# Performance work log

Hardware: AMD Instinct MI355X
Metric: run time of the kernel (lower is better)

The kernel has to match this reference:

```python
import jax, jax.numpy as jnp
import numpy as np

E = 16          # total experts (two halves of 8)
E_HALF = 8
K = 2           # top-k per token
CAP_FACTOR = 2  # expert capacity factor over the average load


def setup_inputs() -> dict:
    key = jax.random.key(0)
    ks = jax.random.split(key, 6)
    N, D, F = 16384, 1024, 1024  # tokens, d_model, d_ff (repo uses d_ff == d_model)
    s = 0.02
    return {
        "moe_inp": jax.random.normal(ks[0], (N, D), jnp.float32),
        "gate_w": jax.random.normal(ks[1], (D, E), jnp.float32) * s,   # gate Linear(d_model, 16)
        "gate_b": jnp.zeros((E,), jnp.float32),
        "route_w": jax.random.normal(ks[2], (D, 1), jnp.float32) * s,  # self.weights Linear(d_model, 1)
        "route_b": jnp.zeros((1,), jnp.float32),
        "W1": jax.random.normal(ks[3], (E, D, F), jnp.float32) * s,    # htoh4 per expert
        "b1": jnp.zeros((E, F), jnp.float32),
        "W2": jax.random.normal(ks[4], (E, F, D), jnp.float32) * s,    # h4toh per expert
        "b2": jnp.zeros((E, D), jnp.float32),
    }


def reference(moe_inp, gate_w, gate_b, route_w, route_b, W1, b1, W2, b2):
    N, D = moe_inp.shape
    # --- gate: logits over 16 experts; half 1 -> experts [0,8), half 2 -> experts [8,16)
    logits = moe_inp @ gate_w + gate_b                       # [N, E]
    val1, idx1 = jax.lax.top_k(logits[:, :E_HALF], K)        # [N, K]
    score1 = jax.nn.softmax(val1, axis=-1)
    val2, idx2 = jax.lax.top_k(logits[:, E_HALF:], K)
    score2 = jax.nn.softmax(val2, axis=-1)
    idx2 = idx2 + E_HALF                                     # shift into second expert range (gate_top_k_idx_2 + 8)
    # --- hard binary split of tokens via sigmoid(Linear(d,1)) > 0.5
    group1 = jax.nn.sigmoid(moe_inp @ route_w + route_b) > 0.5   # [N, 1]
    idx = jnp.where(group1, idx1, idx2)                      # [N, K] combined routing
    score = jnp.where(group1, score1, score2)                # [N, K]
    # --- dispatch: flatten (token, slot) pairs, capacity-bucket per expert
    T = N * K
    C = CAP_FACTOR * T // E                                  # expert capacity
    flat_idx = idx.reshape(-1)                               # [T]
    flat_x = jnp.repeat(moe_inp, K, axis=0)                  # [T, D]
    onehot = jax.nn.one_hot(flat_idx, E, dtype=jnp.int32)    # [T, E]
    pos_in_e = (jnp.cumsum(onehot, axis=0) * onehot).sum(axis=1) - 1  # [T] slot within expert
    valid = pos_in_e < C
    safe_pos = jnp.where(valid, pos_in_e, 0)
    buf = jnp.zeros((E, C, D), moe_inp.dtype).at[flat_idx, safe_pos].add(
        jnp.where(valid[:, None], flat_x, 0.0))              # [E, C, D] contiguous per-expert inputs
    # --- grouped expert FFN: relu(x W1 + b1) W2 + b2 (dropout = identity in eval)
    h = jax.nn.relu(jnp.einsum('ecd,edf->ecf', buf, W1) + b1[:, None, :])
    y = jnp.einsum('ecf,efd->ecd', h, W2) + b2[:, None, :]   # [E, C, D]
    # --- gather back and combine with gate scores
    y_flat = jnp.where(valid[:, None], y[flat_idx, safe_pos], 0.0)   # [T, D]
    out = (y_flat.reshape(N, K, D) * score[..., None]).sum(axis=1)   # [N, D]
    return out
```

## Files before the change

kernel.cpp:

```cpp
#include <hip/hip_runtime.h>
#include <hip/hip_bf16.h>
#include <stdint.h>

#define N_TOK 16384
#define DMODEL 1024
#define EXP 16
#define CAP 4096
#define TT 32768

typedef __bf16 bf16x8 __attribute__((ext_vector_type(8)));
typedef __bf16 bf16x4 __attribute__((ext_vector_type(4)));
typedef float  f32x4  __attribute__((ext_vector_type(4)));

__device__ __forceinline__ void gl_lds16(const void* g, void* s) {
  __builtin_amdgcn_global_load_lds(
      (__attribute__((address_space(1))) void*)(void*)g,
      (__attribute__((address_space(3))) void*)s, 16, 0, 0);
}

__device__ __forceinline__ float bfbits2f(unsigned short u) {
  return __uint_as_float(((unsigned)u) << 16);
}

#define FENCE asm volatile("" ::: "memory")
#define BAR() do { FENCE; __builtin_amdgcn_s_barrier(); FENCE; } while (0)

__global__ __launch_bounds__(256) void convw_kernel(const float* __restrict__ W1,
                                                    const float* __restrict__ W2,
                                                    __bf16* __restrict__ W1bt,
                                                    __bf16* __restrict__ W2bt) {
  __shared__ float tile[64][65];
  int b = blockIdx.x;
  int tx = b & 15;
  int ty = (b >> 4) & 15;
  int e  = (b >> 8) & 15;
  int which = (b >> 12) & 1;
  const float* src = (which ? W2 : W1) + (size_t)e * DMODEL * DMODEL;
  __bf16*      dst = (which ? W2bt : W1bt) + (size_t)e * DMODEL * DMODEL;
  int t = threadIdx.x;
  int r = t >> 2;
  int cs = (t & 3) * 16;
  int r0 = ty * 64, c0 = tx * 64;
  #pragma unroll
  for (int i = 0; i < 16; i += 4) {
    float4 v = *(const float4*)(src + (size_t)(r0 + r) * DMODEL + c0 + cs + i);
    tile[r][cs + i + 0] = v.x; tile[r][cs + i + 1] = v.y;
    tile[r][cs + i + 2] = v.z; tile[r][cs + i + 3] = v.w;
  }
  __syncthreads();
  bf16x8 o1, o2;
  #pragma unroll
  for (int i = 0; i < 8; i++) o1[i] = (__bf16)tile[cs + i][r];
  #pragma unroll
  for (int i = 0; i < 8; i++) o2[i] = (__bf16)tile[cs + 8 + i][r];
  *(bf16x8*)(dst + (size_t)(c0 + r) * DMODEL + r0 + cs)     = o1;
  *(bf16x8*)(dst + (size_t)(c0 + r) * DMODEL + r0 + cs + 8) = o2;
}

__global__ __launch_bounds__(256) void gate_kernel(const float* __restrict__ x,
                                                   const float* __restrict__ gw,
                                                   const float* __restrict__ gb,
                                                   const float* __restrict__ rw,
                                                   const float* __restrict__ rb,
                                                   int* __restrict__ idxo,
                                                   float* __restrict__ sco,
                                                   __bf16* __restrict__ Xb) {
  __shared__ float gws[512 * 17];
  __shared__ float rws[512];
  int tid = threadIdx.x;
  int w = tid >> 6, lane = tid & 63;
  int n = blockIdx.x * 4 + w;
  const float* xr = x + (size_t)n * DMODEL;
  __bf16* xbr = Xb + (size_t)n * DMODEL;

  float acc[17];
  #pragma unroll
  for (int j = 0; j < 17; j++) acc[j] = 0.f;

  for (int c = 0; c < 2; c++) {
    int c0 = c * 512;
    __syncthreads();
    for (int i = tid; i < 512 * 16; i += 256)
      gws[(i >> 4) * 17 + (i & 15)] = gw[c0 * 16 + i];
    for (int i = tid; i < 512; i += 256)
      rws[i] = rw[c0 + i];
    __syncthreads();

    float xv[8];
    #pragma unroll
    for (int u = 0; u < 8; u++) xv[u] = xr[c0 + u * 64 + lane];
    #pragma unroll
    for (int u = 0; u < 8; u++) xbr[c0 + u * 64 + lane] = (__bf16)xv[u];
    #pragma unroll
    for (int u = 0; u < 8; u++) {
      int dl = u * 64 + lane;
      const float* g = &gws[dl * 17];
      #pragma unroll
      for (int j = 0; j < 16; j++) acc[j] += xv[u] * g[j];
      acc[16] += xv[u] * rws[dl];
    }
  }

  #pragma unroll
  for (int o = 1; o < 64; o <<= 1) {
    #pragma unroll
    for (int j = 0; j < 17; j++) acc[j] += __shfl_xor(acc[j], o);
  }
  if (lane == 0) {
    float rv = acc[16] + rb[0];
    bool g1 = rv > 0.f;
    float c[8];
    #pragma unroll
    for (int j = 0; j < 8; j++)
      c[j] = (g1 ? acc[j] + gb[j] : acc[8 + j] + gb[8 + j]);
    int i1 = 0; float v1 = c[0];
    #pragma unroll
    for (int j = 1; j < 8; j++) { if (c[j] > v1) { v1 = c[j]; i1 = j; } }
    int i2 = -1; float v2 = -3.4e38f;
    #pragma unroll
    for (int j = 0; j < 8; j++) { if (j != i1 && c[j] > v2) { v2 = c[j]; i2 = j; } }
    float e2 = expf(v2 - v1);
    float den = 1.f + e2;
    int base = g1 ? 0 : 8;
    idxo[2 * n] = base + i1; idxo[2 * n + 1] = base + i2;
    sco[2 * n] = 1.f / den;  sco[2 * n + 1] = e2 / den;
  }
}

__global__ __launch_bounds__(1024) void scan_kernel(const int* __restrict__ idx,
                                                    float* __restrict__ sco,
                                                    int* __restrict__ rowlist,
                                                    int* __restrict__ cnt,
                                                    int* __restrict__ off) {
  __shared__ int hist[16 * 1024];
  int tid = threadIdx.x;
  #pragma unroll
  for (int e = 0; e < 16; e++) hist[e * 1024 + tid] = 0;
  __syncthreads();
  int base = tid * 32;
  for (int i = 0; i < 32; i++) {
    int e = idx[base + i];
    hist[e * 1024 + tid]++;
  }
  __syncthreads();
  int w = tid >> 6, lane = tid & 63;
  {
    int e = w;
    int running = 0;
    for (int cch = 0; cch < 16; cch++) {
      int v = hist[e * 1024 + cch * 64 + lane];
      int orig = v;
      #pragma unroll
      for (int o = 1; o < 64; o <<= 1) {
        int nv = __shfl_up(v, o);
        if (lane >= o) v += nv;
      }
      hist[e * 1024 + cch * 64 + lane] = running + v - orig;
      running += __shfl(v, 63);
    }
    if (lane == 0) cnt[e] = running;
  }
  __syncthreads();
  if (tid == 0) {
    int o = 0;
    for (int e = 0; e < 16; e++) {
      int c = cnt[e]; if (c > CAP) c = CAP;
      off[e] = o; cnt[e] = c; o += c;
    }
  }
  __syncthreads();
  for (int i = 0; i < 32; i++) {
    int t = base + i;
    int e = idx[t];
    int r = hist[e * 1024 + tid]++;
    if (r < CAP) rowlist[e * CAP + r] = t;
    else sco[t] = 0.f;
  }
}

#define GBM 256
#define GBN 256
#define GBK 64
#define NKT (DMODEL / GBK)

__global__ __launch_bounds__(512) void moe_gemm(const __bf16* __restrict__ A,
                                                const __bf16* __restrict__ Bt,
                                                const float* __restrict__ bias,
                                                __bf16* __restrict__ out,
                                                const int* __restrict__ rowlist,
                                                const int* __restrict__ cnt,
                                                const int* __restrict__ off,
                                                int mode) {
  __shared__ char lds[131072];
  int bx = blockIdx.x;
  int em = (bx & 7) * 32 + (bx >> 3);
  int e  = em >> 4;
  int m0 = (em & 15) * GBM;
  int ce = cnt[e];
  if (m0 >= ce) return;
  int n0 = blockIdx.y * GBN;
  int oe = off[e];
  int tid = threadIdx.x;

  const __bf16* aP[2][2];
  const __bf16* bP[2][2];
  #pragma unroll
  for (int h = 0; h < 2; h++)
    #pragma unroll
    for (int j = 0; j < 2; j++) {
      int lin = j * 512 + tid;
      int srow = lin >> 3;
      int gsrc = (lin & 7) ^ (srow & 7);
      int rr = m0 + h * 128 + srow; if (rr > ce - 1) rr = ce - 1;
      size_t arow;
      if (mode == 0) arow = (size_t)(rowlist[e * CAP + rr] >> 1);
      else           arow = (size_t)(oe + rr);
      aP[h][j] = A + arow * DMODEL + gsrc * 8;
      bP[h][j] = Bt + (size_t)e * DMODEL * DMODEL + (size_t)(n0 + h * 128 + srow) * DMODEL + gsrc * 8;
    }

  int w = tid >> 6, lane = tid & 63;
  int ah = w >> 2;
  int bh = (w & 3) >> 1;
  int bl = (w & 1) * 64;
  int fr = lane & 15, fg = lane >> 4;

  int aRd = ah * 16384 + fr * 128;
  int bRd = 65536 + bh * 16384 + (bl + fr) * 128;
  int gk0 = ((fg)     ^ (fr & 7)) * 16;
  int gk1 = ((4 | fg) ^ (fr & 7)) * 16;

  f32x4 acc[8][4];
  #pragma unroll
  for (int mi = 0; mi < 8; mi++)
    #pragma unroll
    for (int ni = 0; ni < 4; ni++)
      #pragma unroll
      for (int l = 0; l < 4; l++) acc[mi][ni][l] = 0.f;

  auto stA = [&](int s, int h) {
    char* dst = lds + (s & 1) * 32768 + h * 16384;
    gl_lds16(aP[h][0] + s * 64, dst + (size_t)tid * 16);
    gl_lds16(aP[h][1] + s * 64, dst + (size_t)(512 + tid) * 16);
  };
  auto stB = [&](int s, int h) {
    char* dst = lds + 65536 + (s & 1) * 32768 + h * 16384;
    gl_lds16(bP[h][0] + s * 64, dst + (size_t)tid * 16);
    gl_lds16(bP[h][1] + s * 64, dst + (size_t)(512 + tid) * 16);
  };

  stA(0, 0); stA(0, 1); stB(0, 0); stB(0, 1);
  stA(1, 0); stA(1, 1); stB(1, 0); stB(1, 1);
  asm volatile("s_waitcnt vmcnt(8)" ::: "memory");
  BAR();

  bf16x8 afA[4][2], bq0[2][2], bq1[2][2];
  for (int t = 0; t < NKT; ++t) {
    const char* Ab = lds + (t & 1) * 32768 + aRd;
    const char* Bb = lds + (t & 1) * 32768 + bRd;

    #pragma unroll
    for (int mi = 0; mi < 4; mi++) {
      afA[mi][0] = *(const bf16x8*)(Ab + mi * 2048 + gk0);
      afA[mi][1] = *(const bf16x8*)(Ab + mi * 2048 + gk1);
    }
    #pragma unroll
    for (int ni = 0; ni < 2; ni++) {
      bq0[ni][0] = *(const bf16x8*)(Bb + ni * 2048 + gk0);
      bq0[ni][1] = *(const bf16x8*)(Bb + ni * 2048 + gk1);
    }
    if (t >= 1 && t <= 14) stA(t + 1, 0);
    BAR();
    __builtin_amdgcn_s_setprio(1);
    #pragma unroll
    for (int kk = 0; kk < 2; kk++)
      #pragma unroll
      for (int mi = 0; mi < 4; mi++)
        #pragma unroll
        for (int ni = 0; ni < 2; ni++)
          acc[mi][ni] = __builtin_amdgcn_mfma_f32_16x16x32_bf16(afA[mi][kk], bq0[ni][kk], acc[mi][ni], 0, 0, 0);
    __builtin_amdgcn_s_setprio(0);
    BAR();

    #pragma unroll
    for (int ni = 0; ni < 2; ni++) {
      bq1[ni][0] = *(const bf16x8*)(Bb + (2 + ni) * 2048 + gk0);
      bq1[ni][1] = *(const bf16x8*)(Bb + (2 + ni) * 2048 + gk1);
    }
    if (t >= 1 && t <= 14) stA(t + 1, 1);
    BAR();
    __builtin_amdgcn_s_setprio(1);
    #pragma unroll
    for (int kk = 0; kk < 2; kk++)
      #pragma unroll
      for (int mi = 0; mi < 4; mi++)
        #pragma unroll
        for (int ni = 0; ni < 2; ni++)
          acc[mi][2 + ni] = __builtin_amdgcn_mfma_f32_16x16x32_bf16(afA[mi][kk], bq1[ni][kk], acc[mi][2 + ni], 0, 0, 0);
    __builtin_amdgcn_s_setprio(0);
    BAR();

    #pragma unroll
    for (int mi = 0; mi < 4; mi++) {
      afA[mi][0] = *(const bf16x8*)(Ab + (4 + mi) * 2048 + gk0);
      afA[mi][1] = *(const bf16x8*)(Ab + (4 + mi) * 2048 + gk1);
    }
    if (t <= 13) stB(t + 2, 0);
    BAR();
    __builtin_amdgcn_s_setprio(1);
    #pragma unroll
    for (int kk = 0; kk < 2; kk++)
      #pragma unroll
      for (int mi = 0; mi < 4; mi++)
        #pragma unroll
        for (int ni = 0; ni < 2; ni++)
          acc[4 + mi][2 + ni] = __builtin_amdgcn_mfma_f32_16x16x32_bf16(afA[mi][kk], bq1[ni][kk], acc[4 + mi][2 + ni], 0, 0, 0);
    __builtin_amdgcn_s_setprio(0);
    BAR();

    if (t <= 13) stB(t + 2, 1);
    BAR();
    __builtin_amdgcn_s_setprio(1);
    #pragma unroll
    for (int kk = 0; kk < 2; kk++)
      #pragma unroll
      for (int mi = 0; mi < 4; mi++)
        #pragma unroll
        for (int ni = 0; ni < 2; ni++)
          acc[4 + mi][ni] = __builtin_amdgcn_mfma_f32_16x16x32_bf16(afA[mi][kk], bq0[ni][kk], acc[4 + mi][ni], 0, 0, 0);
    __builtin_amdgcn_s_setprio(0);
    if (t <= 13)      asm volatile("s_waitcnt vmcnt(4)" ::: "memory");
    else if (t == 14) asm volatile("s_waitcnt vmcnt(0)" ::: "memory");
    BAR();
  }

  int wr = ah * 128, wc = (w & 3) * 64;
  float bcol[4];
  #pragma unroll
  for (int ni = 0; ni < 4; ni++)
    bcol[ni] = bias[(size_t)e * DMODEL + n0 + wc + ni * 16 + fr];
  #pragma unroll
  for (int mi = 0; mi < 8; mi++) {
    #pragma unroll
    for (int r = 0; r < 4; r++) {
      int grow = m0 + wr + mi * 16 + fg * 4 + r;
      if (grow >= ce) continue;
      size_t orow = (mode == 0) ? (size_t)(oe + grow)
                                : (size_t)rowlist[e * CAP + grow];
      __bf16* op = out + orow * DMODEL + n0 + wc + fr;
      #pragma unroll
      for (int ni = 0; ni < 4; ni++) {
        float v = acc[mi][ni][r] + bcol[ni];
        if (mode == 0) v = fmaxf(v, 0.f);
        op[ni * 16] = (__bf16)v;
      }
    }
  }
}

__global__ __launch_bounds__(256) void combine_kernel(const __bf16* __restrict__ y,
                                                      const float* __restrict__ sco,
                                                      float* __restrict__ out) {
  int n = blockIdx.x;
  int d = threadIdx.x * 4;
  float s0 = sco[2 * n], s1 = sco[2 * n + 1];
  ushort4 a = *(const ushort4*)((const unsigned short*)(y + (size_t)(2 * n) * DMODEL + d));
  ushort4 b = *(const ushort4*)((const unsigned short*)(y + (size_t)(2 * n + 1) * DMODEL + d));
  float4 o;
  o.x = s0 * bfbits2f(a.x) + s1 * bfbits2f(b.x);
  o.y = s0 * bfbits2f(a.y) + s1 * bfbits2f(b.y);
  o.z = s0 * bfbits2f(a.z) + s1 * bfbits2f(b.z);
  o.w = s0 * bfbits2f(a.w) + s1 * bfbits2f(b.w);
  *(float4*)(out + (size_t)n * DMODEL + d) = o;
}

extern "C" void kernel_launch(void* const* d_in, const int* in_sizes, int n_in,
                              void* d_out, int out_size, void* d_ws, size_t ws_size,
                              hipStream_t stream) {
  const float* moe = (const float*)d_in[0];
  const float* gw  = (const float*)d_in[1];
  const float* gb  = (const float*)d_in[2];
  const float* rw  = (const float*)d_in[3];
  const float* rb  = (const float*)d_in[4];
  const float* W1  = (const float*)d_in[5];
  const float* b1  = (const float*)d_in[6];
  const float* W2  = (const float*)d_in[7];
  const float* b2  = (const float*)d_in[8];
  float* out = (float*)d_out;

  char* p = (char*)d_ws;
  __bf16* Xb   = (__bf16*)p; p += (size_t)N_TOK * DMODEL * 2;
  __bf16* W1bt = (__bf16*)p; p += (size_t)EXP * DMODEL * DMODEL * 2;
  __bf16* W2bt = (__bf16*)p; p += (size_t)EXP * DMODEL * DMODEL * 2;
  __bf16* hbuf = (__bf16*)p; p += (size_t)TT * DMODEL * 2;
  __bf16* ybuf = (__bf16*)p; p += (size_t)TT * DMODEL * 2;
  int*   idxb   = (int*)p;   p += (size_t)TT * 4;
  float* scoreb = (float*)p; p += (size_t)TT * 4;
  int*   rowlist = (int*)p;  p += (size_t)EXP * CAP * 4;
  int*   cntb    = (int*)p;  p += 64;
  int*   offb    = (int*)p;  p += 64;

  convw_kernel<<<dim3(8192), dim3(256), 0, stream>>>(W1, W2, W1bt, W2bt);
  gate_kernel<<<dim3(4096), dim3(256), 0, stream>>>(moe, gw, gb, rw, rb, idxb, scoreb, Xb);
  scan_kernel<<<dim3(1), dim3(1024), 0, stream>>>(idxb, scoreb, rowlist, cntb, offb);
  moe_gemm<<<dim3(256, 4), dim3(512), 0, stream>>>(Xb, W1bt, b1, hbuf, rowlist, cntb, offb, 0);
  moe_gemm<<<dim3(256, 4), dim3(512), 0, stream>>>(hbuf, W2bt, b2, ybuf, rowlist, cntb, offb, 1);
  combine_kernel<<<dim3(16384), dim3(256), 0, stream>>>(ybuf, scoreb, out);
}
```

Measured before the change: 411.0 us.

## Use 16 waves per GEMM block with 64x64 per-wave tiles

The expert GEMM now runs 1024-thread blocks, so 16 waves each own a 64x64 sub-tile of the 256x256 output instead of 8 waves each owning a 128x64 region. The loads are reorganised to match: each thread issues two 16-byte global-to-LDS loads per operand, and the per-iteration schedule drops from four MFMA phases to two, prefetching A and B two stages ahead. The aim is more waves to hide latency and fewer accumulator registers per wave. In exchange each wave reads more LDS data per MFMA, and the larger block adds barrier overhead. The launch_bounds minimum-block hint of 4 cannot be met with 128KB of LDS per block.

```diff
diff --git a/kernel.cpp b/kernel.cpp
--- a/kernel.cpp
+++ b/kernel.cpp
@@ -183,14 +183,14 @@
 #define GBK 64
 #define NKT (DMODEL / GBK)
 
-__global__ __launch_bounds__(512) void moe_gemm(const __bf16* __restrict__ A,
-                                                const __bf16* __restrict__ Bt,
-                                                const float* __restrict__ bias,
-                                                __bf16* __restrict__ out,
-                                                const int* __restrict__ rowlist,
-                                                const int* __restrict__ cnt,
-                                                const int* __restrict__ off,
-                                                int mode) {
+__global__ __launch_bounds__(1024, 4) void moe_gemm(const __bf16* __restrict__ A,
+                                                    const __bf16* __restrict__ Bt,
+                                                    const float* __restrict__ bias,
+                                                    __bf16* __restrict__ out,
+                                                    const int* __restrict__ rowlist,
+                                                    const int* __restrict__ cnt,
+                                                    const int* __restrict__ off,
+                                                    int mode) {
   __shared__ char lds[131072];
   int bx = blockIdx.x;
   int em = (bx & 7) * 32 + (bx >> 3);
@@ -202,56 +202,52 @@
   int oe = off[e];
   int tid = threadIdx.x;
 
-  const __bf16* aP[2][2];
-  const __bf16* bP[2][2];
-  #pragma unroll
-  for (int h = 0; h < 2; h++)
-    #pragma unroll
-    for (int j = 0; j < 2; j++) {
-      int lin = j * 512 + tid;
-      int srow = lin >> 3;
-      int gsrc = (lin & 7) ^ (srow & 7);
-      int rr = m0 + h * 128 + srow; if (rr > ce - 1) rr = ce - 1;
-      size_t arow;
-      if (mode == 0) arow = (size_t)(rowlist[e * CAP + rr] >> 1);
-      else           arow = (size_t)(oe + rr);
-      aP[h][j] = A + arow * DMODEL + gsrc * 8;
-      bP[h][j] = Bt + (size_t)e * DMODEL * DMODEL + (size_t)(n0 + h * 128 + srow) * DMODEL + gsrc * 8;
-    }
+  const __bf16* aP[2];
+  const __bf16* bP[2];
+  #pragma unroll
+  for (int j = 0; j < 2; j++) {
+    int c = j * 1024 + tid;
+    int srow = c >> 3;
+    int gsrc = (c & 7) ^ (srow & 7);
+    int rr = m0 + srow; if (rr > ce - 1) rr = ce - 1;
+    size_t arow;
+    if (mode == 0) arow = (size_t)(rowlist[e * CAP + rr] >> 1);
+    else           arow = (size_t)(oe + rr);
+    aP[j] = A + arow * DMODEL + gsrc * 8;
+    bP[j] = Bt + (size_t)e * DMODEL * DMODEL + (size_t)(n0 + srow) * DMODEL + gsrc * 8;
+  }
 
   int w = tid >> 6, lane = tid & 63;
-  int ah = w >> 2;
-  int bh = (w & 3) >> 1;
-  int bl = (w & 1) * 64;
+  int wr = (w >> 2) * 64;
+  int wc = (w & 3) * 64;
   int fr = lane & 15, fg = lane >> 4;
 
-  int aRd = ah * 16384 + fr * 128;
-  int bRd = 65536 + bh * 16384 + (bl + fr) * 128;
+  int aRd = wr * 128 + fr * 128;
+  int bRd = 65536 + wc * 128 + fr * 128;
   int gk0 = ((fg)     ^ (fr & 7)) * 16;
   int gk1 = ((4 | fg) ^ (fr & 7)) * 16;
 
-  f32x4 acc[8][4];
-  #pragma unroll
-  for (int mi = 0; mi < 8; mi++)
+  f32x4 acc[4][4];
+  #pragma unroll
+  for (int mi = 0; mi < 4; mi++)
     #pragma unroll
     for (int ni = 0; ni < 4; ni++)
       #pragma unroll
       for (int l = 0; l < 4; l++) acc[mi][ni][l] = 0.f;
 
-  auto stA = [&](int s, int h) {
-    char* dst = lds + (s & 1) * 32768 + h * 16384;
-    gl_lds16(aP[h][0] + s * 64, dst + (size_t)tid * 16);
-    gl_lds16(aP[h][1] + s * 64, dst + (size_t)(512 + tid) * 16);
+  auto stA = [&](int s) {
+    char* dst = lds + (s & 1) * 32768;
+    gl_lds16(aP[0] + s * 64, dst + (size_t)tid * 16);
+    gl_lds16(aP[1] + s * 64, dst + (size_t)(1024 + tid) * 16);
   };
-  auto stB = [&](int s, int h) {
-    char* dst = lds + 65536 + (s & 1) * 32768 + h * 16384;
-    gl_lds16(bP[h][0] + s * 64, dst + (size_t)tid * 16);
-    gl_lds16(bP[h][1] + s * 64, dst + (size_t)(512 + tid) * 16);
+  auto stB = [&](int s) {
+    char* dst = lds + 65536 + (s & 1) * 32768;
+    gl_lds16(bP[0] + s * 64, dst + (size_t)tid * 16);
+    gl_lds16(bP[1] + s * 64, dst + (size_t)(1024 + tid) * 16);
   };
 
-  stA(0, 0); stA(0, 1); stB(0, 0); stB(0, 1);
-  stA(1, 0); stA(1, 1); stB(1, 0); stB(1, 1);
-  asm volatile("s_waitcnt vmcnt(8)" ::: "memory");
+  stA(0); stB(0); stA(1); stB(1);
+  asm volatile("s_waitcnt vmcnt(4)" ::: "memory");
   BAR();
 
   bf16x8 afA[4][2], bq0[2][2], bq1[2][2];
@@ -269,7 +265,7 @@
       bq0[ni][0] = *(const bf16x8*)(Bb + ni * 2048 + gk0);
       bq0[ni][1] = *(const bf16x8*)(Bb + ni * 2048 + gk1);
     }
-    if (t >= 1 && t <= 14) stA(t + 1, 0);
+    if (t <= 13) stA(t + 2);
     BAR();
     __builtin_amdgcn_s_setprio(1);
     #pragma unroll
@@ -287,7 +283,7 @@
       bq1[ni][0] = *(const bf16x8*)(Bb + (2 + ni) * 2048 + gk0);
       bq1[ni][1] = *(const bf16x8*)(Bb + (2 + ni) * 2048 + gk1);
     }
-    if (t >= 1 && t <= 14) stA(t + 1, 1);
+    if (t <= 13) stB(t + 2);
     BAR();
     __builtin_amdgcn_s_setprio(1);
     #pragma unroll
@@ -298,49 +294,17 @@
         for (int ni = 0; ni < 2; ni++)
           acc[mi][2 + ni] = __builtin_amdgcn_mfma_f32_16x16x32_bf16(afA[mi][kk], bq1[ni][kk], acc[mi][2 + ni], 0, 0, 0);
     __builtin_amdgcn_s_setprio(0);
-    BAR();
-
-    #pragma unroll
-    for (int mi = 0; mi < 4; mi++) {
-      afA[mi][0] = *(const bf16x8*)(Ab + (4 + mi) * 2048 + gk0);
-      afA[mi][1] = *(const bf16x8*)(Ab + (4 + mi) * 2048 + gk1);
-    }
-    if (t <= 13) stB(t + 2, 0);
-    BAR();
-    __builtin_amdgcn_s_setprio(1);
-    #pragma unroll
-    for (int kk = 0; kk < 2; kk++)
-      #pragma unroll
-      for (int mi = 0; mi < 4; mi++)
-        #pragma unroll
-        for (int ni = 0; ni < 2; ni++)
-          acc[4 + mi][2 + ni] = __builtin_amdgcn_mfma_f32_16x16x32_bf16(afA[mi][kk], bq1[ni][kk], acc[4 + mi][2 + ni], 0, 0, 0);
-    __builtin_amdgcn_s_setprio(0);
-    BAR();
-
-    if (t <= 13) stB(t + 2, 1);
-    BAR();
-    __builtin_amdgcn_s_setprio(1);
-    #pragma unroll
-    for (int kk = 0; kk < 2; kk++)
-      #pragma unroll
-      for (int mi = 0; mi < 4; mi++)
-        #pragma unroll
-        for (int ni = 0; ni < 2; ni++)
-          acc[4 + mi][ni] = __builtin_amdgcn_mfma_f32_16x16x32_bf16(afA[mi][kk], bq0[ni][kk], acc[4 + mi][ni], 0, 0, 0);
-    __builtin_amdgcn_s_setprio(0);
     if (t <= 13)      asm volatile("s_waitcnt vmcnt(4)" ::: "memory");
     else if (t == 14) asm volatile("s_waitcnt vmcnt(0)" ::: "memory");
     BAR();
   }
 
-  int wr = ah * 128, wc = (w & 3) * 64;
   float bcol[4];
   #pragma unroll
   for (int ni = 0; ni < 4; ni++)
     bcol[ni] = bias[(size_t)e * DMODEL + n0 + wc + ni * 16 + fr];
   #pragma unroll
-  for (int mi = 0; mi < 8; mi++) {
+  for (int mi = 0; mi < 4; mi++) {
     #pragma unroll
     for (int r = 0; r < 4; r++) {
       int grow = m0 + wr + mi * 16 + fg * 4 + r;
@@ -403,7 +367,7 @@
   convw_kernel<<<dim3(8192), dim3(256), 0, stream>>>(W1, W2, W1bt, W2bt);
   gate_kernel<<<dim3(4096), dim3(256), 0, stream>>>(moe, gw, gb, rw, rb, idxb, scoreb, Xb);
   scan_kernel<<<dim3(1), dim3(1024), 0, stream>>>(idxb, scoreb, rowlist, cntb, offb);
-  moe_gemm<<<dim3(256, 4), dim3(512), 0, stream>>>(Xb, W1bt, b1, hbuf, rowlist, cntb, offb, 0);
-  moe_gemm<<<dim3(256, 4), dim3(512), 0, stream>>>(hbuf, W2bt, b2, ybuf, rowlist, cntb, offb, 1);
+  moe_gemm<<<dim3(256, 4), dim3(1024), 0, stream>>>(Xb, W1bt, b1, hbuf, rowlist, cntb, offb, 0);
+  moe_gemm<<<dim3(256, 4), dim3(1024), 0, stream>>>(hbuf, W2bt, b2, ybuf, rowlist, cntb, offb, 1);
   combine_kernel<<<dim3(16384), dim3(256), 0, stream>>>(ybuf, scoreb, out);
 }
```

Measured after the change: 446.4 us. 8.6% more time.
